# Kernel optimization log

Hardware: AMD Instinct MI355X
Metric: run time of the kernel (lower is better)

The kernel has to match this reference:

```python
import jax, jax.numpy as jnp
import numpy as np

U, B, I, D = 50000, 20000, 40000, 64
E_UI, E_UB, E_UBX, E_AGG = 1000000, 600000, 800000, 300000
EPS = 1e-8


def _bip_graph(rng, nA, nB, nE):
    """Symmetric Laplacian-normalized bipartite graph as directed COO edge list."""
    r = rng.integers(0, nA, nE)
    c = rng.integers(0, nB, nE)
    deg_r = np.bincount(r, minlength=nA).astype(np.float32)
    deg_c = np.bincount(c, minlength=nB).astype(np.float32)
    v = (1.0 / (np.sqrt(deg_r[r]) + EPS)) * (1.0 / (np.sqrt(deg_c[c]) + EPS))
    rows = np.concatenate([r, c + nA])
    cols = np.concatenate([c + nA, r])
    vals = np.concatenate([v, v]).astype(np.float32)
    return np.stack([rows, cols]).astype(np.int32), vals


def setup_inputs() -> dict:
    rng = np.random.default_rng(0)
    ui_idx, ui_val = _bip_graph(rng, U, I, E_UI)
    ub_idx, ub_val = _bip_graph(rng, U, B, E_UB)
    ubx_idx, ubx_val = _bip_graph(rng, U, B, E_UBX)  # ingredient-augmented u-b graph
    # bundle aggregation graph: row-normalized B x I (bi graph)
    br = rng.integers(0, B, E_AGG)
    bc = rng.integers(0, I, E_AGG)
    bdeg = np.bincount(br, minlength=B).astype(np.float32)
    agg_val = (1.0 / np.maximum(bdeg[br], 1.0)).astype(np.float32)
    agg_idx = np.stack([br, bc]).astype(np.int32)
    key = jax.random.key(0)
    ku, kb, ki = jax.random.split(key, 3)
    s = np.sqrt(2.0 / (U + D)).astype(np.float32)  # xavier-normal-ish scale
    return {
        "users_feature": jax.random.normal(ku, (U, D), jnp.float32) * 0.02,
        "bundles_feature": jax.random.normal(kb, (B, D), jnp.float32) * 0.02,
        "items_feature": jax.random.normal(ki, (I, D), jnp.float32) * 0.02,
        "ui_idx": jnp.asarray(ui_idx), "ui_val": jnp.asarray(ui_val),
        "ub_idx": jnp.asarray(ub_idx), "ub_val": jnp.asarray(ub_val),
        "ubx_idx": jnp.asarray(ubx_idx), "ubx_val": jnp.asarray(ubx_val),
        "agg_idx": jnp.asarray(agg_idx), "agg_val": jnp.asarray(agg_val),
        "num_layers": 2,
    }


def _spmm(idx, val, x, n_out):
    # y[r] += val[e] * x[c] for each edge e=(r,c)
    return jax.ops.segment_sum(val[:, None] * x[idx[1]], idx[0], num_segments=n_out)


def _l2norm(x):
    n = jnp.sqrt(jnp.sum(x * x, axis=1, keepdims=True))
    return x / jnp.maximum(n, 1e-12)


def _one_propagate(idx, val, A_feat, B_feat, num_layers):
    feats = jnp.concatenate([A_feat, B_feat], axis=0)
    n = feats.shape[0]
    acc = feats  # layer 0 raw
    f = feats
    for i in range(num_layers):
        f = _spmm(idx, val, f, n) / (i + 2)
        acc = acc + _l2norm(f)
    return acc[: A_feat.shape[0]], acc[A_feat.shape[0]:]


def reference(users_feature, bundles_feature, items_feature, ui_idx, ui_val,
              ub_idx, ub_val, ubx_idx, ubx_val, agg_idx, agg_val, num_layers):
    # item-level propagation over user-item graph
    IL_u, IL_i = _one_propagate(ui_idx, ui_val, users_feature, items_feature, num_layers)
    IL_b = _spmm(agg_idx, agg_val, IL_i, bundles_feature.shape[0])  # bundle agg from items
    # bundle-level propagation over user-bundle graph
    BL_u, BL_b = _one_propagate(ub_idx, ub_val, users_feature, bundles_feature, num_layers)
    # ingredient-augmented user-bundle propagation
    XL_u, XL_b = _one_propagate(ubx_idx, ubx_val, users_feature, bundles_feature, num_layers)
    # pack all representations: [3*U + 3*B, D]
    return jnp.concatenate([IL_u, BL_u, XL_u, IL_b, BL_b, XL_b], axis=0)
```

## Files before the change

kernel.cpp:

```cpp
#include <hip/hip_runtime.h>

#define D 64
constexpr int U_ = 50000, B_ = 20000, I_ = 40000;
constexpr int RPB  = 128;
constexpr int MAXB = 708;
constexpr int PTILE = 8192;

constexpr int NBU = 390;
constexpr int CAPU_UI = 3584, CAPB_UI = 4352;
constexpr int CAPA    = 2560;
constexpr int CAPU_UB = 2432, CAPB_UB = 4864;
constexpr int CAPU_UX = 2944, CAPB_UX = 6272;

__device__ __forceinline__ int g_nbU(int seg) { return seg == 1 ? 0 : NBU; }
__device__ __forceinline__ int g_capU(int seg) {
    switch (seg) { case 0: return CAPU_UI; case 1: return CAPA;
                   case 2: return CAPU_UB; default: return CAPU_UX; }
}
__device__ __forceinline__ int g_capB(int seg) {
    switch (seg) { case 0: return CAPB_UI; case 1: return CAPA;
                   case 2: return CAPB_UB; default: return CAPB_UX; }
}
__device__ __forceinline__ int bbase(int seg, int b) {
    int nbU = g_nbU(seg);
    return (b <= nbU) ? b * g_capU(seg)
                      : nbU * g_capU(seg) + (b - nbU) * g_capB(seg);
}

__device__ __forceinline__ unsigned short f2bf(float f) {
    unsigned int u = __float_as_uint(f);
    return (unsigned short)((u + 0x7FFFu + ((u >> 16) & 1u)) >> 16);
}

struct BuildP {
    const int *r0, *r1, *r2, *r3;
    int nnz0, nnz1, nnz2, nnz3;
    int G0, G1, G2, G3;
    int nb0, nb1, nb2, nb3;
    int co0, co1, co2, co3;
};

__global__ void __launch_bounds__(256)
k_cnt4(BuildP p, int* __restrict__ cnt) {
    __shared__ int lcnt[MAXB];
    int blk = blockIdx.x, t = threadIdx.x;
    int seg, rel, nnz, G, nbuck, co; const int* rows;
    if (blk < p.G0)                   { seg=0; rel=blk;              rows=p.r0; nnz=p.nnz0; G=p.G0; nbuck=p.nb0; co=p.co0; }
    else if (blk < p.G0+p.G1)         { seg=1; rel=blk-p.G0;         rows=p.r1; nnz=p.nnz1; G=p.G1; nbuck=p.nb1; co=p.co1; }
    else if (blk < p.G0+p.G1+p.G2)    { seg=2; rel=blk-p.G0-p.G1;    rows=p.r2; nnz=p.nnz2; G=p.G2; nbuck=p.nb2; co=p.co2; }
    else                              { seg=3; rel=blk-p.G0-p.G1-p.G2; rows=p.r3; nnz=p.nnz3; G=p.G3; nbuck=p.nb3; co=p.co3; }
    (void)seg;
    for (int i = t; i < nbuck; i += 256) lcnt[i] = 0;
    __syncthreads();
    int e0 = rel * PTILE, e1 = min(e0 + PTILE, nnz);
    int e = e0 + t;
    for (; e + 1792 < e1; e += 2048) {
        int r[8];
        #pragma unroll
        for (int k = 0; k < 8; k++) r[k] = rows[e + k * 256];
        #pragma unroll
        for (int k = 0; k < 8; k++) atomicAdd(&lcnt[r[k] >> 7], 1);
    }
    for (; e < e1; e += 256) atomicAdd(&lcnt[rows[e] >> 7], 1);
    __syncthreads();
    for (int b = t; b < nbuck; b += 256) cnt[co + (size_t)b * G + rel] = lcnt[b];
}

__global__ void __launch_bounds__(256)
k_scan4(BuildP p, int* __restrict__ cnt, int* __restrict__ bktcur) {
    __shared__ int sv[256];
    int bk = blockIdx.x, t = threadIdx.x;
    int seg, rel, G, co;
    if (bk < p.nb0)                    { seg=0; rel=bk;                 G=p.G0; co=p.co0; }
    else if (bk < p.nb0+p.nb1)         { seg=1; rel=bk-p.nb0;           G=p.G1; co=p.co1; }
    else if (bk < p.nb0+p.nb1+p.nb2)   { seg=2; rel=bk-p.nb0-p.nb1;     G=p.G2; co=p.co2; }
    else                               { seg=3; rel=bk-p.nb0-p.nb1-p.nb2; G=p.G3; co=p.co3; }
    int x = (t < G) ? cnt[co + (size_t)rel * G + t] : 0;
    sv[t] = x;
    __syncthreads();
    for (int off = 1; off < 256; off <<= 1) {
        int y = (t >= off) ? sv[t - off] : 0;
        __syncthreads();
        sv[t] += y;
        __syncthreads();
    }
    int bb = bbase(seg, rel);
    if (t < G) cnt[co + (size_t)rel * G + t] = bb + sv[t] - x;
    if (t == 255) bktcur[seg * MAXB + rel] = bb + sv[255];
}

__global__ void __launch_bounds__(256)
k_scat(const int* __restrict__ rows, const int* __restrict__ cols,
       int nnz, int G, int nbuck, int seg,
       const int* __restrict__ cnt, int* __restrict__ ep) {
    __shared__ int lbase[MAXB], lcnt[MAXB], llim[MAXB];
    int t = threadIdx.x, blk = blockIdx.x;
    for (int b = t; b < nbuck; b += 256) {
        lbase[b] = cnt[(size_t)b * G + blk];
        llim[b]  = bbase(seg, b + 1);
        lcnt[b]  = 0;
    }
    __syncthreads();
    int e0 = blk * PTILE, e1 = min(e0 + PTILE, nnz);
    int e = e0 + t;
    for (; e + 1792 < e1; e += 2048) {
        int r[8], c[8];
        #pragma unroll
        for (int k = 0; k < 8; k++) { r[k] = rows[e + k * 256]; c[k] = cols[e + k * 256]; }
        #pragma unroll
        for (int k = 0; k < 8; k++) {
            int b = r[k] >> 7;
            int pos = lbase[b] + atomicAdd(&lcnt[b], 1);
            if (pos < llim[b])
                ep[pos] = ((r[k] & (RPB - 1)) << 17) | c[k];
        }
    }
    for (; e < e1; e += 256) {
        int r = rows[e], c = cols[e];
        int b = r >> 7;
        int pos = lbase[b] + atomicAdd(&lcnt[b], 1);
        if (pos < llim[b])
            ep[pos] = ((r & (RPB - 1)) << 17) | c;
    }
}

__global__ void __launch_bounds__(256)
k_sort(const int* __restrict__ ep, const int* __restrict__ bktcur, int seg,
       int n, int mode, int do_pad, int* __restrict__ ecolS,
       int* __restrict__ rowstart, int* __restrict__ rowend,
       float* __restrict__ scale, int do_stage,
       const float* __restrict__ rawA, const float* __restrict__ rawB_adj,
       ushort* __restrict__ fb) {
    __shared__ int lc[4 * 129];
    __shared__ float sscale[RPB];
    __shared__ int wtot;
    int t = threadIdx.x;
    int b = blockIdx.x;
    int s = bbase(seg, b);
    int e = min(bktcur[b], bbase(seg, b + 1));
    int ne = e - s;
    for (int i = t; i < 4 * 129; i += 256) lc[i] = 0;
    __syncthreads();
    int rep = (t & 3) * 129;
    int i = t;
    for (; i + 768 < ne; i += 1024) {
        int p0 = ep[s + i], p1 = ep[s + i + 256], p2 = ep[s + i + 512], p3 = ep[s + i + 768];
        atomicAdd(&lc[rep + (p0 >> 17)], 1); atomicAdd(&lc[rep + (p1 >> 17)], 1);
        atomicAdd(&lc[rep + (p2 >> 17)], 1); atomicAdd(&lc[rep + (p3 >> 17)], 1);
    }
    for (; i < ne; i += 256) { int p = ep[s + i]; atomicAdd(&lc[rep + (p >> 17)], 1); }
    __syncthreads();
    int c_t = 0, pc_t = 0, v = 0;
    if (t < RPB) {
        c_t = lc[t] + lc[129 + t] + lc[258 + t] + lc[387 + t];
        pc_t = do_pad ? ((c_t + 7) & ~7) : c_t;
        v = pc_t;
        for (int off = 1; off < 64; off <<= 1) {
            int y = __shfl_up(v, off, 64);
            if ((t & 63) >= off) v += y;
        }
    }
    if (t == 63) wtot = v;
    __syncthreads();
    if (t >= 64 && t < RPB) v += wtot;
    if (t < RPB) {
        int row = b * RPB + t;
        if (row < n) {
            int st = s + (v - pc_t);
            rowstart[row] = st;
            rowend[row]   = st + pc_t;
            float sc = (mode == 0) ? 1.0f / (sqrtf((float)c_t) + 1e-8f)
                                   : 1.0f / (float)max(c_t, 1);
            scale[row] = sc;
            sscale[t] = sc;
            for (int k = c_t; k < pc_t; k++) ecolS[st + k] = n;
            lc[t] = st;
        } else lc[t] = 0;
    }
    __syncthreads();
    i = t;
    for (; i + 768 < ne; i += 1024) {
        int p0 = ep[s + i], p1 = ep[s + i + 256], p2 = ep[s + i + 512], p3 = ep[s + i + 768];
        int q0 = atomicAdd(&lc[p0 >> 17], 1); ecolS[q0] = p0 & 0x1FFFF;
        int q1 = atomicAdd(&lc[p1 >> 17], 1); ecolS[q1] = p1 & 0x1FFFF;
        int q2 = atomicAdd(&lc[p2 >> 17], 1); ecolS[q2] = p2 & 0x1FFFF;
        int q3 = atomicAdd(&lc[p3 >> 17], 1); ecolS[q3] = p3 & 0x1FFFF;
    }
    for (; i < ne; i += 256) {
        int p = ep[s + i];
        int q = atomicAdd(&lc[p >> 17], 1);
        ecolS[q] = p & 0x1FFFF;
    }
    if (do_stage) {
        int r0 = b * RPB;
        for (int idx = t; idx < RPB * 16; idx += 256) {
            int rl = idx >> 4, q = idx & 15;
            int row = r0 + rl;
            if (row > n) continue;
            ushort4 o;
            if (row == n) {
                o = make_ushort4(0, 0, 0, 0);
            } else {
                float sc = sscale[rl];
                float4 vv = (row < U_) ? ((const float4*)rawA)[(size_t)row * 16 + q]
                                       : ((const float4*)rawB_adj)[(size_t)row * 16 + q];
                o.x = f2bf(vv.x * sc); o.y = f2bf(vv.y * sc);
                o.z = f2bf(vv.z * sc); o.w = f2bf(vv.w * sc);
            }
            ((ushort4*)fb)[(size_t)row * 16 + q] = o;
        }
    }
}

__global__ void __launch_bounds__(256)
k_layer(const int* __restrict__ rowstart, const int* __restrict__ rowend,
        const int* __restrict__ ecol,
        const float* __restrict__ scale, int n, int zrow,
        const ushort* __restrict__ x, float inv,
        const float* __restrict__ rawA, const float* __restrict__ rawB_adj,
        ushort* __restrict__ fout, int write_f, int init,
        float* __restrict__ accA, float* __restrict__ accB) {
    if (write_f && blockIdx.x == 0 && threadIdx.x < 16)
        ((ushort4*)(fout + ((size_t)zrow << 6)))[threadIdx.x] = make_ushort4(0, 0, 0, 0);
    const int lane = threadIdx.x & 63;
    const int qtr  = lane >> 4;
    const int ql   = lane & 15;
    const int g = ql >> 3, q = ql & 7;
    int rowA = (blockIdx.x << 4) + ((threadIdx.x >> 6) << 2);
    if (rowA >= n) return;
    int row = rowA + qtr;
    int s = 0, e = 0;
    if (row < n) { s = rowstart[row]; e = rowend[row]; }
    float a0=0.f,a1=0.f,a2=0.f,a3=0.f,a4=0.f,a5=0.f,a6=0.f,a7=0.f;
    const uint4* __restrict__ xb = (const uint4*)x;

#define LDQ(m, vv) { int c_ = __shfl(cj, (qtr << 4) + ((m) << 1) + g, 64); \
                     vv = xb[((size_t)(unsigned)c_ << 3) + (unsigned)q]; }
#define ACCQ(vv) { \
    a0 += __uint_as_float(vv.x << 16); a1 += __uint_as_float(vv.x & 0xFFFF0000u); \
    a2 += __uint_as_float(vv.y << 16); a3 += __uint_as_float(vv.y & 0xFFFF0000u); \
    a4 += __uint_as_float(vv.z << 16); a5 += __uint_as_float(vv.z & 0xFFFF0000u); \
    a6 += __uint_as_float(vv.w << 16); a7 += __uint_as_float(vv.w & 0xFFFF0000u); }

    for (int base = s; base < e; base += 16) {
        int jn = e - base;
        int cj = ecol[base + ql];
        uint4 v0, v1, v2, v3, v4, v5, v6, v7;
        if (jn >= 16) {
            LDQ(0, v0); LDQ(1, v1); LDQ(2, v2); LDQ(3, v3);
            LDQ(4, v4); ACCQ(v0);
            LDQ(5, v5); ACCQ(v1);
            LDQ(6, v6); ACCQ(v2);
            LDQ(7, v7); ACCQ(v3);
            ACCQ(v4); ACCQ(v5); ACCQ(v6); ACCQ(v7);
        } else {
            LDQ(0, v0); LDQ(1, v1); LDQ(2, v2); LDQ(3, v3);
            ACCQ(v0); ACCQ(v1); ACCQ(v2); ACCQ(v3);
        }
    }
#undef LDQ
#undef ACCQ
#define RED(aa) { aa += __shfl_xor(aa, 8, 64); }
    RED(a0) RED(a1) RED(a2) RED(a3) RED(a4) RED(a5) RED(a6) RED(a7)
#undef RED
    float srow = (row < n) ? scale[row] : 0.f;
    float mlt = srow * inv;
    float w0=a0*mlt, w1=a1*mlt, w2=a2*mlt, w3=a3*mlt;
    float w4=a4*mlt, w5=a5*mlt, w6=a6*mlt, w7=a7*mlt;
    float sq = w0*w0 + w1*w1 + w2*w2 + w3*w3 + w4*w4 + w5*w5 + w6*w6 + w7*w7;
    sq += __shfl_xor(sq, 1, 64); sq += __shfl_xor(sq, 2, 64); sq += __shfl_xor(sq, 4, 64);
    float rn = 1.0f / fmaxf(sqrtf(sq), 1e-12f);
    if (row < n && g == 0) {
        size_t o = ((size_t)row << 6) + ((unsigned)q << 3);
        if (write_f) {
            unsigned p0 = (unsigned)f2bf(w0*srow) | ((unsigned)f2bf(w1*srow) << 16);
            unsigned p1 = (unsigned)f2bf(w2*srow) | ((unsigned)f2bf(w3*srow) << 16);
            unsigned p2 = (unsigned)f2bf(w4*srow) | ((unsigned)f2bf(w5*srow) << 16);
            unsigned p3 = (unsigned)f2bf(w6*srow) | ((unsigned)f2bf(w7*srow) << 16);
            *(uint4*)(fout + o) = make_uint4(p0, p1, p2, p3);
        }
        float r0=w0*rn, r1=w1*rn, r2=w2*rn, r3=w3*rn;
        float r4=w4*rn, r5=w5*rn, r6=w6*rn, r7=w7*rn;
        float* p = (row < U_) ? accA + o : accB + (o - ((size_t)U_ << 6));
        float4 c0, c1;
        if (init) {
            const float4* rp = (const float4*)((row < U_) ? rawA : rawB_adj)
                               + ((size_t)row << 4) + ((unsigned)q << 1);
            c0 = rp[0]; c1 = rp[1];
        } else {
            c0 = ((const float4*)p)[0]; c1 = ((const float4*)p)[1];
        }
        ((float4*)p)[0] = make_float4(c0.x + r0, c0.y + r1, c0.z + r2, c0.w + r3);
        ((float4*)p)[1] = make_float4(c1.x + r4, c1.y + r5, c1.z + r6, c1.w + r7);
    }
}

__global__ void k_spmm_csr(const int* __restrict__ rowstart, const int* __restrict__ rowend,
                           const int* __restrict__ ecol,
                           const float* __restrict__ rs, int n,
                           const float* __restrict__ x, float* __restrict__ y) {
    int row = (blockIdx.x << 2) + (threadIdx.x >> 6);
    if (row >= n) return;
    int lane = threadIdx.x & 63;
    int s = rowstart[row], e = rowend[row];
    float acc = 0.f;
    for (int base = s; base < e; base += 64) {
        int jn = e - base; if (jn > 64) jn = 64;
        int li = base + (lane < jn ? lane : jn - 1);
        int cj = ecol[li];
        int j = 0;
        for (; j + 8 <= jn; j += 8) {
            int c0 = __shfl(cj, j + 0, 64), c1 = __shfl(cj, j + 1, 64);
            int c2 = __shfl(cj, j + 2, 64), c3 = __shfl(cj, j + 3, 64);
            int c4 = __shfl(cj, j + 4, 64), c5 = __shfl(cj, j + 5, 64);
            int c6 = __shfl(cj, j + 6, 64), c7 = __shfl(cj, j + 7, 64);
            float v0 = x[(size_t)c0 * D + lane], v1 = x[(size_t)c1 * D + lane];
            float v2 = x[(size_t)c2 * D + lane], v3 = x[(size_t)c3 * D + lane];
            float v4 = x[(size_t)c4 * D + lane], v5 = x[(size_t)c5 * D + lane];
            float v6 = x[(size_t)c6 * D + lane], v7 = x[(size_t)c7 * D + lane];
            acc += ((v0 + v1) + (v2 + v3)) + ((v4 + v5) + (v6 + v7));
        }
        for (; j < jn; j++) {
            int c = __shfl(cj, j, 64);
            acc += x[(size_t)c * D + lane];
        }
    }
    y[(size_t)row * D + lane] = acc * rs[row];
}

extern "C" void kernel_launch(void* const* d_in, const int* in_sizes, int n_in,
                              void* d_out, int out_size, void* d_ws, size_t ws_size,
                              hipStream_t stream) {
    const float* users   = (const float*)d_in[0];
    const float* bundles = (const float*)d_in[1];
    const float* items   = (const float*)d_in[2];
    const int*   ui_idx  = (const int*)d_in[3];
    const int*   ub_idx  = (const int*)d_in[5];
    const int*   ubx_idx = (const int*)d_in[7];
    const int*   agg_idx = (const int*)d_in[9];
    const int ui_nnz  = in_sizes[4];
    const int ub_nnz  = in_sizes[6];
    const int ubx_nnz = in_sizes[8];
    const int agg_nnz = in_sizes[10];

    float* out = (float*)d_out;
    const size_t rowf = (size_t)D;

    const int NROWPAD = 90004;
    const int EPMAX   = 547 * 6144;
    ushort* fb16    = (ushort*)d_ws;
    float*  acc_itm = (float*)(fb16 + (size_t)(90001) * D + 32);
    float*  scale   = acc_itm + (size_t)I_ * D;
    int*    ep      = (int*)(scale + NROWPAD);
    ushort* gb16    = (ushort*)ep;
    int*    ecolS   = ep + EPMAX;
    int*    rowstart= ecolS + EPMAX;
    int*    rowend  = rowstart + NROWPAD;
    int*    bktcur  = rowend + NROWPAD;
    int*    cnt     = ep + 2950000;

    float* out_IL_u = out;
    float* out_BL_u = out + (size_t)U_ * rowf;
    float* out_XL_u = out + (size_t)2 * U_ * rowf;
    float* out_IL_b = out + (size_t)3 * U_ * rowf;
    float* out_BL_b = out + (size_t)3 * U_ * rowf + (size_t)B_ * rowf;
    float* out_XL_b = out + (size_t)3 * U_ * rowf + (size_t)2 * B_ * rowf;

    BuildP P;
    P.r0 = ui_idx;  P.nnz0 = ui_nnz;  P.G0 = (ui_nnz  + PTILE - 1) / PTILE;  P.nb0 = 704;
    P.r1 = agg_idx; P.nnz1 = agg_nnz; P.G1 = (agg_nnz + PTILE - 1) / PTILE;  P.nb1 = 157;
    P.r2 = ub_idx;  P.nnz2 = ub_nnz;  P.G2 = (ub_nnz  + PTILE - 1) / PTILE;  P.nb2 = 547;
    P.r3 = ubx_idx; P.nnz3 = ubx_nnz; P.G3 = (ubx_nnz + PTILE - 1) / PTILE;  P.nb3 = 547;
    P.co0 = 0;
    P.co1 = P.co0 + P.nb0 * P.G0;
    P.co2 = P.co1 + P.nb1 * P.G1;
    P.co3 = P.co2 + P.nb2 * P.G2;
    int Gsum  = P.G0 + P.G1 + P.G2 + P.G3;
    int nbsum = P.nb0 + P.nb1 + P.nb2 + P.nb3;
    hipLaunchKernelGGL(k_cnt4,  dim3(Gsum),  dim3(256), 0, stream, P, cnt);
    hipLaunchKernelGGL(k_scan4, dim3(nbsum), dim3(256), 0, stream, P, cnt, bktcur);

    auto build = [&](const int* idxp, int nnz, int n, int mode, int do_pad,
                     int do_stage, const float* A, const float* Badj,
                     int seg, int G, int co) {
        int nbuck = (n + RPB - 1) / RPB;
        hipLaunchKernelGGL(k_scat, dim3(G), dim3(256), 0, stream,
                           idxp, idxp + nnz, nnz, G, nbuck, seg, cnt + co, ep);
        hipLaunchKernelGGL(k_sort, dim3(nbuck), dim3(256), 0, stream,
                           ep, bktcur + seg * MAXB, seg, n, mode, do_pad, ecolS,
                           rowstart, rowend, scale, do_stage, A, Badj, fb16);
    };

    auto propagate = [&](const int* idxp, int nnz, int seg, int G, int co,
                         const float* Bfeat, int nB, float* accA, float* accB) {
        const int n = U_ + nB;
        const float* Badj = Bfeat - (size_t)U_ * rowf;
        build(idxp, nnz, n, 0, 1, 1, users, Badj, seg, G, co);
        hipLaunchKernelGGL(k_layer, dim3((n + 15) / 16), dim3(256), 0, stream,
                           rowstart, rowend, ecolS, scale, n, n, fb16, 0.5f,
                           users, Badj, gb16, 1, 1, accA, accB);
        hipLaunchKernelGGL(k_layer, dim3((n + 15) / 16), dim3(256), 0, stream,
                           rowstart, rowend, ecolS, scale, n, n, gb16, 1.0f / 3.0f,
                           users, Badj, (ushort*)nullptr, 0, 0, accA, accB);
    };

    propagate(ui_idx, ui_nnz, 0, P.G0, P.co0, items, I_, out_IL_u, acc_itm);

    build(agg_idx, agg_nnz, B_, 1, 0, 0, users, users, 1, P.G1, P.co1);
    hipLaunchKernelGGL(k_spmm_csr, dim3((B_ + 3) / 4), dim3(256), 0, stream,
                       rowstart, rowend, ecolS, scale, B_, acc_itm, out_IL_b);

    propagate(ub_idx, ub_nnz, 2, P.G2, P.co2, bundles, B_, out_BL_u, out_BL_b);

    propagate(ubx_idx, ubx_nnz, 3, P.G3, P.co3, bundles, B_, out_XL_u, out_XL_b);
}
```

Before: 463.3 us.

## Fuse graph build and propagation phases into persistent cooperative kernels

Replaces the many per-stage kernel launches (count, scan, scatter, sort, two layers, spmm) with two cooperative persistent kernels that loop over work with grid-stride blocks and separate phases with grid-wide syncs. The aim is to remove launch overhead and inter-kernel gaps across the roughly fourteen launches. In exchange, grid size is capped by occupancy, so each block processes several logical blocks serially. Grid syncs carry their own cost, and the fused kernel may use more registers, lowering occupancy for the layer phase.

New measurement: 1.747 ms. 277% more time.

```diff
diff --git a/kernel.cpp b/kernel.cpp
--- a/kernel.cpp
+++ b/kernel.cpp
@@ -1,4 +1,7 @@
 #include <hip/hip_runtime.h>
+#include <hip/hip_cooperative_groups.h>
+
+namespace cg = cooperative_groups;
 
 #define D 64
 constexpr int U_ = 50000, B_ = 20000, I_ = 40000;
@@ -41,199 +44,90 @@
 };
 
 __global__ void __launch_bounds__(256)
-k_cnt4(BuildP p, int* __restrict__ cnt) {
+k_cntscan(BuildP p, int* cnt, int* bktcur) {
+    cg::grid_group gg = cg::this_grid();
     __shared__ int lcnt[MAXB];
-    int blk = blockIdx.x, t = threadIdx.x;
-    int seg, rel, nnz, G, nbuck, co; const int* rows;
-    if (blk < p.G0)                   { seg=0; rel=blk;              rows=p.r0; nnz=p.nnz0; G=p.G0; nbuck=p.nb0; co=p.co0; }
-    else if (blk < p.G0+p.G1)         { seg=1; rel=blk-p.G0;         rows=p.r1; nnz=p.nnz1; G=p.G1; nbuck=p.nb1; co=p.co1; }
-    else if (blk < p.G0+p.G1+p.G2)    { seg=2; rel=blk-p.G0-p.G1;    rows=p.r2; nnz=p.nnz2; G=p.G2; nbuck=p.nb2; co=p.co2; }
-    else                              { seg=3; rel=blk-p.G0-p.G1-p.G2; rows=p.r3; nnz=p.nnz3; G=p.G3; nbuck=p.nb3; co=p.co3; }
-    (void)seg;
-    for (int i = t; i < nbuck; i += 256) lcnt[i] = 0;
-    __syncthreads();
-    int e0 = rel * PTILE, e1 = min(e0 + PTILE, nnz);
-    int e = e0 + t;
-    for (; e + 1792 < e1; e += 2048) {
-        int r[8];
-        #pragma unroll
-        for (int k = 0; k < 8; k++) r[k] = rows[e + k * 256];
-        #pragma unroll
-        for (int k = 0; k < 8; k++) atomicAdd(&lcnt[r[k] >> 7], 1);
-    }
-    for (; e < e1; e += 256) atomicAdd(&lcnt[rows[e] >> 7], 1);
-    __syncthreads();
-    for (int b = t; b < nbuck; b += 256) cnt[co + (size_t)b * G + rel] = lcnt[b];
-}
-
-__global__ void __launch_bounds__(256)
-k_scan4(BuildP p, int* __restrict__ cnt, int* __restrict__ bktcur) {
     __shared__ int sv[256];
-    int bk = blockIdx.x, t = threadIdx.x;
-    int seg, rel, G, co;
-    if (bk < p.nb0)                    { seg=0; rel=bk;                 G=p.G0; co=p.co0; }
-    else if (bk < p.nb0+p.nb1)         { seg=1; rel=bk-p.nb0;           G=p.G1; co=p.co1; }
-    else if (bk < p.nb0+p.nb1+p.nb2)   { seg=2; rel=bk-p.nb0-p.nb1;     G=p.G2; co=p.co2; }
-    else                               { seg=3; rel=bk-p.nb0-p.nb1-p.nb2; G=p.G3; co=p.co3; }
-    int x = (t < G) ? cnt[co + (size_t)rel * G + t] : 0;
-    sv[t] = x;
-    __syncthreads();
-    for (int off = 1; off < 256; off <<= 1) {
-        int y = (t >= off) ? sv[t - off] : 0;
+    int t = threadIdx.x;
+    int Gsum = p.G0 + p.G1 + p.G2 + p.G3;
+    for (int blk = blockIdx.x; blk < Gsum; blk += gridDim.x) {
+        int rel, nnz, G, nbuck, co; const int* rows;
+        if (blk < p.G0)                   { rel=blk;                 rows=p.r0; nnz=p.nnz0; G=p.G0; nbuck=p.nb0; co=p.co0; }
+        else if (blk < p.G0+p.G1)         { rel=blk-p.G0;            rows=p.r1; nnz=p.nnz1; G=p.G1; nbuck=p.nb1; co=p.co1; }
+        else if (blk < p.G0+p.G1+p.G2)    { rel=blk-p.G0-p.G1;       rows=p.r2; nnz=p.nnz2; G=p.G2; nbuck=p.nb2; co=p.co2; }
+        else                              { rel=blk-p.G0-p.G1-p.G2;  rows=p.r3; nnz=p.nnz3; G=p.G3; nbuck=p.nb3; co=p.co3; }
         __syncthreads();
-        sv[t] += y;
+        for (int i = t; i < nbuck; i += 256) lcnt[i] = 0;
         __syncthreads();
-    }
-    int bb = bbase(seg, rel);
-    if (t < G) cnt[co + (size_t)rel * G + t] = bb + sv[t] - x;
-    if (t == 255) bktcur[seg * MAXB + rel] = bb + sv[255];
-}
-
-__global__ void __launch_bounds__(256)
-k_scat(const int* __restrict__ rows, const int* __restrict__ cols,
-       int nnz, int G, int nbuck, int seg,
-       const int* __restrict__ cnt, int* __restrict__ ep) {
-    __shared__ int lbase[MAXB], lcnt[MAXB], llim[MAXB];
-    int t = threadIdx.x, blk = blockIdx.x;
-    for (int b = t; b < nbuck; b += 256) {
-        lbase[b] = cnt[(size_t)b * G + blk];
-        llim[b]  = bbase(seg, b + 1);
-        lcnt[b]  = 0;
-    }
-    __syncthreads();
-    int e0 = blk * PTILE, e1 = min(e0 + PTILE, nnz);
-    int e = e0 + t;
-    for (; e + 1792 < e1; e += 2048) {
-        int r[8], c[8];
-        #pragma unroll
-        for (int k = 0; k < 8; k++) { r[k] = rows[e + k * 256]; c[k] = cols[e + k * 256]; }
-        #pragma unroll
-        for (int k = 0; k < 8; k++) {
-            int b = r[k] >> 7;
-            int pos = lbase[b] + atomicAdd(&lcnt[b], 1);
-            if (pos < llim[b])
-                ep[pos] = ((r[k] & (RPB - 1)) << 17) | c[k];
-        }
-    }
-    for (; e < e1; e += 256) {
-        int r = rows[e], c = cols[e];
-        int b = r >> 7;
-        int pos = lbase[b] + atomicAdd(&lcnt[b], 1);
-        if (pos < llim[b])
-            ep[pos] = ((r & (RPB - 1)) << 17) | c;
-    }
-}
-
-__global__ void __launch_bounds__(256)
-k_sort(const int* __restrict__ ep, const int* __restrict__ bktcur, int seg,
-       int n, int mode, int do_pad, int* __restrict__ ecolS,
-       int* __restrict__ rowstart, int* __restrict__ rowend,
-       float* __restrict__ scale, int do_stage,
-       const float* __restrict__ rawA, const float* __restrict__ rawB_adj,
-       ushort* __restrict__ fb) {
-    __shared__ int lc[4 * 129];
-    __shared__ float sscale[RPB];
-    __shared__ int wtot;
-    int t = threadIdx.x;
-    int b = blockIdx.x;
-    int s = bbase(seg, b);
-    int e = min(bktcur[b], bbase(seg, b + 1));
-    int ne = e - s;
-    for (int i = t; i < 4 * 129; i += 256) lc[i] = 0;
-    __syncthreads();
-    int rep = (t & 3) * 129;
-    int i = t;
-    for (; i + 768 < ne; i += 1024) {
-        int p0 = ep[s + i], p1 = ep[s + i + 256], p2 = ep[s + i + 512], p3 = ep[s + i + 768];
-        atomicAdd(&lc[rep + (p0 >> 17)], 1); atomicAdd(&lc[rep + (p1 >> 17)], 1);
-        atomicAdd(&lc[rep + (p2 >> 17)], 1); atomicAdd(&lc[rep + (p3 >> 17)], 1);
-    }
-    for (; i < ne; i += 256) { int p = ep[s + i]; atomicAdd(&lc[rep + (p >> 17)], 1); }
-    __syncthreads();
-    int c_t = 0, pc_t = 0, v = 0;
-    if (t < RPB) {
-        c_t = lc[t] + lc[129 + t] + lc[258 + t] + lc[387 + t];
-        pc_t = do_pad ? ((c_t + 7) & ~7) : c_t;
-        v = pc_t;
-        for (int off = 1; off < 64; off <<= 1) {
-            int y = __shfl_up(v, off, 64);
-            if ((t & 63) >= off) v += y;
-        }
-    }
-    if (t == 63) wtot = v;
-    __syncthreads();
-    if (t >= 64 && t < RPB) v += wtot;
-    if (t < RPB) {
-        int row = b * RPB + t;
-        if (row < n) {
-            int st = s + (v - pc_t);
-            rowstart[row] = st;
-            rowend[row]   = st + pc_t;
-            float sc = (mode == 0) ? 1.0f / (sqrtf((float)c_t) + 1e-8f)
-                                   : 1.0f / (float)max(c_t, 1);
-            scale[row] = sc;
-            sscale[t] = sc;
-            for (int k = c_t; k < pc_t; k++) ecolS[st + k] = n;
-            lc[t] = st;
-        } else lc[t] = 0;
-    }
-    __syncthreads();
-    i = t;
-    for (; i + 768 < ne; i += 1024) {
-        int p0 = ep[s + i], p1 = ep[s + i + 256], p2 = ep[s + i + 512], p3 = ep[s + i + 768];
-        int q0 = atomicAdd(&lc[p0 >> 17], 1); ecolS[q0] = p0 & 0x1FFFF;
-        int q1 = atomicAdd(&lc[p1 >> 17], 1); ecolS[q1] = p1 & 0x1FFFF;
-        int q2 = atomicAdd(&lc[p2 >> 17], 1); ecolS[q2] = p2 & 0x1FFFF;
-        int q3 = atomicAdd(&lc[p3 >> 17], 1); ecolS[q3] = p3 & 0x1FFFF;
-    }
-    for (; i < ne; i += 256) {
-        int p = ep[s + i];
-        int q = atomicAdd(&lc[p >> 17], 1);
-        ecolS[q] = p & 0x1FFFF;
-    }
-    if (do_stage) {
-        int r0 = b * RPB;
-        for (int idx = t; idx < RPB * 16; idx += 256) {
-            int rl = idx >> 4, q = idx & 15;
-            int row = r0 + rl;
-            if (row > n) continue;
-            ushort4 o;
-            if (row == n) {
-                o = make_ushort4(0, 0, 0, 0);
-            } else {
-                float sc = sscale[rl];
-                float4 vv = (row < U_) ? ((const float4*)rawA)[(size_t)row * 16 + q]
-                                       : ((const float4*)rawB_adj)[(size_t)row * 16 + q];
-                o.x = f2bf(vv.x * sc); o.y = f2bf(vv.y * sc);
-                o.z = f2bf(vv.z * sc); o.w = f2bf(vv.w * sc);
-            }
-            ((ushort4*)fb)[(size_t)row * 16 + q] = o;
-        }
-    }
-}
-
-__global__ void __launch_bounds__(256)
-k_layer(const int* __restrict__ rowstart, const int* __restrict__ rowend,
-        const int* __restrict__ ecol,
-        const float* __restrict__ scale, int n, int zrow,
-        const ushort* __restrict__ x, float inv,
-        const float* __restrict__ rawA, const float* __restrict__ rawB_adj,
-        ushort* __restrict__ fout, int write_f, int init,
-        float* __restrict__ accA, float* __restrict__ accB) {
+        int e0 = rel * PTILE, e1 = min(e0 + PTILE, nnz);
+        int e = e0 + t;
+        for (; e + 1792 < e1; e += 2048) {
+            int r[8];
+            #pragma unroll
+            for (int k = 0; k < 8; k++) r[k] = rows[e + k * 256];
+            #pragma unroll
+            for (int k = 0; k < 8; k++) atomicAdd(&lcnt[r[k] >> 7], 1);
+        }
+        for (; e < e1; e += 256) atomicAdd(&lcnt[rows[e] >> 7], 1);
+        __syncthreads();
+        for (int b = t; b < nbuck; b += 256) cnt[co + (size_t)b * G + rel] = lcnt[b];
+    }
+    gg.sync();
+    int nbsum = p.nb0 + p.nb1 + p.nb2 + p.nb3;
+    for (int bk = blockIdx.x; bk < nbsum; bk += gridDim.x) {
+        int seg, rel, G, co;
+        if (bk < p.nb0)                    { seg=0; rel=bk;                   G=p.G0; co=p.co0; }
+        else if (bk < p.nb0+p.nb1)         { seg=1; rel=bk-p.nb0;             G=p.G1; co=p.co1; }
+        else if (bk < p.nb0+p.nb1+p.nb2)   { seg=2; rel=bk-p.nb0-p.nb1;       G=p.G2; co=p.co2; }
+        else                               { seg=3; rel=bk-p.nb0-p.nb1-p.nb2; G=p.G3; co=p.co3; }
+        int x = (t < G) ? cnt[co + (size_t)rel * G + t] : 0;
+        __syncthreads();
+        sv[t] = x;
+        __syncthreads();
+        for (int off = 1; off < 256; off <<= 1) {
+            int y = (t >= off) ? sv[t - off] : 0;
+            __syncthreads();
+            sv[t] += y;
+            __syncthreads();
+        }
+        int bb = bbase(seg, rel);
+        if (t < G) cnt[co + (size_t)rel * G + t] = bb + sv[t] - x;
+        if (t == 255) bktcur[seg * MAXB + rel] = bb + sv[255];
+    }
+}
+
+struct GP {
+    const int* rows; const int* cols;
+    const int* cnt;
+    int* ep;
+    const int* bktcur;
+    int* ecolS; int* rowstart; int* rowend; float* scale;
+    const float* rawA; const float* rawB_adj;
+    ushort* fb; ushort* gb;
+    float* accA; float* accB;
+    const float* spx; float* spy;
+    float inv0, inv1;
+    int nnz, G, nbuck, seg, n, mode, do_pad, do_stage, do_layers, do_spmm, spn;
+};
+
+__device__ __forceinline__ void layer_phase(const GP& P, const ushort* x,
+                                            ushort* fout, float inv,
+                                            int write_f, int init) {
     if (write_f && blockIdx.x == 0 && threadIdx.x < 16)
-        ((ushort4*)(fout + ((size_t)zrow << 6)))[threadIdx.x] = make_ushort4(0, 0, 0, 0);
+        ((ushort4*)(fout + ((size_t)P.n << 6)))[threadIdx.x] = make_ushort4(0, 0, 0, 0);
     const int lane = threadIdx.x & 63;
     const int qtr  = lane >> 4;
     const int ql   = lane & 15;
     const int g = ql >> 3, q = ql & 7;
-    int rowA = (blockIdx.x << 4) + ((threadIdx.x >> 6) << 2);
-    if (rowA >= n) return;
-    int row = rowA + qtr;
-    int s = 0, e = 0;
-    if (row < n) { s = rowstart[row]; e = rowend[row]; }
-    float a0=0.f,a1=0.f,a2=0.f,a3=0.f,a4=0.f,a5=0.f,a6=0.f,a7=0.f;
-    const uint4* __restrict__ xb = (const uint4*)x;
-
+    const uint4* xb = (const uint4*)x;
+    int nq = (P.n + 15) >> 4;
+    for (int blk = blockIdx.x; blk < nq; blk += gridDim.x) {
+        int rowA = (blk << 4) + ((threadIdx.x >> 6) << 2);
+        if (rowA >= P.n) continue;
+        int row = rowA + qtr;
+        int s = 0, e = 0;
+        if (row < P.n) { s = P.rowstart[row]; e = P.rowend[row]; }
+        float a0=0.f,a1=0.f,a2=0.f,a3=0.f,a4=0.f,a5=0.f,a6=0.f,a7=0.f;
 #define LDQ(m, vv) { int c_ = __shfl(cj, (qtr << 4) + ((m) << 1) + g, 64); \
                      vv = xb[((size_t)(unsigned)c_ << 3) + (unsigned)q]; }
 #define ACCQ(vv) { \
@@ -241,91 +135,220 @@
     a2 += __uint_as_float(vv.y << 16); a3 += __uint_as_float(vv.y & 0xFFFF0000u); \
     a4 += __uint_as_float(vv.z << 16); a5 += __uint_as_float(vv.z & 0xFFFF0000u); \
     a6 += __uint_as_float(vv.w << 16); a7 += __uint_as_float(vv.w & 0xFFFF0000u); }
-
-    for (int base = s; base < e; base += 16) {
-        int jn = e - base;
-        int cj = ecol[base + ql];
-        uint4 v0, v1, v2, v3, v4, v5, v6, v7;
-        if (jn >= 16) {
-            LDQ(0, v0); LDQ(1, v1); LDQ(2, v2); LDQ(3, v3);
-            LDQ(4, v4); ACCQ(v0);
-            LDQ(5, v5); ACCQ(v1);
-            LDQ(6, v6); ACCQ(v2);
-            LDQ(7, v7); ACCQ(v3);
-            ACCQ(v4); ACCQ(v5); ACCQ(v6); ACCQ(v7);
-        } else {
-            LDQ(0, v0); LDQ(1, v1); LDQ(2, v2); LDQ(3, v3);
-            ACCQ(v0); ACCQ(v1); ACCQ(v2); ACCQ(v3);
-        }
-    }
+        for (int base = s; base < e; base += 16) {
+            int jn = e - base;
+            int cj = P.ecolS[base + ql];
+            uint4 v0, v1, v2, v3, v4, v5, v6, v7;
+            if (jn >= 16) {
+                LDQ(0, v0); LDQ(1, v1); LDQ(2, v2); LDQ(3, v3);
+                LDQ(4, v4); ACCQ(v0);
+                LDQ(5, v5); ACCQ(v1);
+                LDQ(6, v6); ACCQ(v2);
+                LDQ(7, v7); ACCQ(v3);
+                ACCQ(v4); ACCQ(v5); ACCQ(v6); ACCQ(v7);
+            } else {
+                LDQ(0, v0); LDQ(1, v1); LDQ(2, v2); LDQ(3, v3);
+                ACCQ(v0); ACCQ(v1); ACCQ(v2); ACCQ(v3);
+            }
+        }
 #undef LDQ
 #undef ACCQ
 #define RED(aa) { aa += __shfl_xor(aa, 8, 64); }
-    RED(a0) RED(a1) RED(a2) RED(a3) RED(a4) RED(a5) RED(a6) RED(a7)
+        RED(a0) RED(a1) RED(a2) RED(a3) RED(a4) RED(a5) RED(a6) RED(a7)
 #undef RED
-    float srow = (row < n) ? scale[row] : 0.f;
-    float mlt = srow * inv;
-    float w0=a0*mlt, w1=a1*mlt, w2=a2*mlt, w3=a3*mlt;
-    float w4=a4*mlt, w5=a5*mlt, w6=a6*mlt, w7=a7*mlt;
-    float sq = w0*w0 + w1*w1 + w2*w2 + w3*w3 + w4*w4 + w5*w5 + w6*w6 + w7*w7;
-    sq += __shfl_xor(sq, 1, 64); sq += __shfl_xor(sq, 2, 64); sq += __shfl_xor(sq, 4, 64);
-    float rn = 1.0f / fmaxf(sqrtf(sq), 1e-12f);
-    if (row < n && g == 0) {
-        size_t o = ((size_t)row << 6) + ((unsigned)q << 3);
-        if (write_f) {
-            unsigned p0 = (unsigned)f2bf(w0*srow) | ((unsigned)f2bf(w1*srow) << 16);
-            unsigned p1 = (unsigned)f2bf(w2*srow) | ((unsigned)f2bf(w3*srow) << 16);
-            unsigned p2 = (unsigned)f2bf(w4*srow) | ((unsigned)f2bf(w5*srow) << 16);
-            unsigned p3 = (unsigned)f2bf(w6*srow) | ((unsigned)f2bf(w7*srow) << 16);
-            *(uint4*)(fout + o) = make_uint4(p0, p1, p2, p3);
-        }
-        float r0=w0*rn, r1=w1*rn, r2=w2*rn, r3=w3*rn;
-        float r4=w4*rn, r5=w5*rn, r6=w6*rn, r7=w7*rn;
-        float* p = (row < U_) ? accA + o : accB + (o - ((size_t)U_ << 6));
-        float4 c0, c1;
-        if (init) {
-            const float4* rp = (const float4*)((row < U_) ? rawA : rawB_adj)
-                               + ((size_t)row << 4) + ((unsigned)q << 1);
-            c0 = rp[0]; c1 = rp[1];
-        } else {
-            c0 = ((const float4*)p)[0]; c1 = ((const float4*)p)[1];
-        }
-        ((float4*)p)[0] = make_float4(c0.x + r0, c0.y + r1, c0.z + r2, c0.w + r3);
-        ((float4*)p)[1] = make_float4(c1.x + r4, c1.y + r5, c1.z + r6, c1.w + r7);
-    }
-}
-
-__global__ void k_spmm_csr(const int* __restrict__ rowstart, const int* __restrict__ rowend,
-                           const int* __restrict__ ecol,
-                           const float* __restrict__ rs, int n,
-                           const float* __restrict__ x, float* __restrict__ y) {
-    int row = (blockIdx.x << 2) + (threadIdx.x >> 6);
-    if (row >= n) return;
+        float srow = (row < P.n) ? P.scale[row] : 0.f;
+        float mlt = srow * inv;
+        float w0=a0*mlt, w1=a1*mlt, w2=a2*mlt, w3=a3*mlt;
+        float w4=a4*mlt, w5=a5*mlt, w6=a6*mlt, w7=a7*mlt;
+        float sq = w0*w0 + w1*w1 + w2*w2 + w3*w3 + w4*w4 + w5*w5 + w6*w6 + w7*w7;
+        sq += __shfl_xor(sq, 1, 64); sq += __shfl_xor(sq, 2, 64); sq += __shfl_xor(sq, 4, 64);
+        float rn = 1.0f / fmaxf(sqrtf(sq), 1e-12f);
+        if (row < P.n && g == 0) {
+            size_t o = ((size_t)row << 6) + ((unsigned)q << 3);
+            if (write_f) {
+                unsigned p0 = (unsigned)f2bf(w0*srow) | ((unsigned)f2bf(w1*srow) << 16);
+                unsigned p1 = (unsigned)f2bf(w2*srow) | ((unsigned)f2bf(w3*srow) << 16);
+                unsigned p2 = (unsigned)f2bf(w4*srow) | ((unsigned)f2bf(w5*srow) << 16);
+                unsigned p3 = (unsigned)f2bf(w6*srow) | ((unsigned)f2bf(w7*srow) << 16);
+                *(uint4*)(fout + o) = make_uint4(p0, p1, p2, p3);
+            }
+            float r0=w0*rn, r1=w1*rn, r2=w2*rn, r3=w3*rn;
+            float r4=w4*rn, r5=w5*rn, r6=w6*rn, r7=w7*rn;
+            float* p = (row < U_) ? P.accA + o : P.accB + (o - ((size_t)U_ << 6));
+            float4 c0, c1;
+            if (init) {
+                const float4* rp = (const float4*)((row < U_) ? P.rawA : P.rawB_adj)
+                                   + ((size_t)row << 4) + ((unsigned)q << 1);
+                c0 = rp[0]; c1 = rp[1];
+            } else {
+                c0 = ((const float4*)p)[0]; c1 = ((const float4*)p)[1];
+            }
+            ((float4*)p)[0] = make_float4(c0.x + r0, c0.y + r1, c0.z + r2, c0.w + r3);
+            ((float4*)p)[1] = make_float4(c1.x + r4, c1.y + r5, c1.z + r6, c1.w + r7);
+        }
+    }
+}
+
+__device__ void spmm_phase(const GP& P) {
     int lane = threadIdx.x & 63;
-    int s = rowstart[row], e = rowend[row];
-    float acc = 0.f;
-    for (int base = s; base < e; base += 64) {
-        int jn = e - base; if (jn > 64) jn = 64;
-        int li = base + (lane < jn ? lane : jn - 1);
-        int cj = ecol[li];
-        int j = 0;
-        for (; j + 8 <= jn; j += 8) {
-            int c0 = __shfl(cj, j + 0, 64), c1 = __shfl(cj, j + 1, 64);
-            int c2 = __shfl(cj, j + 2, 64), c3 = __shfl(cj, j + 3, 64);
-            int c4 = __shfl(cj, j + 4, 64), c5 = __shfl(cj, j + 5, 64);
-            int c6 = __shfl(cj, j + 6, 64), c7 = __shfl(cj, j + 7, 64);
-            float v0 = x[(size_t)c0 * D + lane], v1 = x[(size_t)c1 * D + lane];
-            float v2 = x[(size_t)c2 * D + lane], v3 = x[(size_t)c3 * D + lane];
-            float v4 = x[(size_t)c4 * D + lane], v5 = x[(size_t)c5 * D + lane];
-            float v6 = x[(size_t)c6 * D + lane], v7 = x[(size_t)c7 * D + lane];
-            acc += ((v0 + v1) + (v2 + v3)) + ((v4 + v5) + (v6 + v7));
-        }
-        for (; j < jn; j++) {
-            int c = __shfl(cj, j, 64);
-            acc += x[(size_t)c * D + lane];
-        }
-    }
-    y[(size_t)row * D + lane] = acc * rs[row];
+    int nb4 = (P.spn + 3) >> 2;
+    for (int blk = blockIdx.x; blk < nb4; blk += gridDim.x) {
+        int row = (blk << 2) + (threadIdx.x >> 6);
+        if (row >= P.spn) continue;
+        int s = P.rowstart[row], e = P.rowend[row];
+        float acc = 0.f;
+        for (int base = s; base < e; base += 64) {
+            int jn = e - base; if (jn > 64) jn = 64;
+            int li = base + (lane < jn ? lane : jn - 1);
+            int cj = P.ecolS[li];
+            int j = 0;
+            for (; j + 8 <= jn; j += 8) {
+                int c0 = __shfl(cj, j + 0, 64), c1 = __shfl(cj, j + 1, 64);
+                int c2 = __shfl(cj, j + 2, 64), c3 = __shfl(cj, j + 3, 64);
+                int c4 = __shfl(cj, j + 4, 64), c5 = __shfl(cj, j + 5, 64);
+                int c6 = __shfl(cj, j + 6, 64), c7 = __shfl(cj, j + 7, 64);
+                float v0 = P.spx[(size_t)c0 * D + lane], v1 = P.spx[(size_t)c1 * D + lane];
+                float v2 = P.spx[(size_t)c2 * D + lane], v3 = P.spx[(size_t)c3 * D + lane];
+                float v4 = P.spx[(size_t)c4 * D + lane], v5 = P.spx[(size_t)c5 * D + lane];
+                float v6 = P.spx[(size_t)c6 * D + lane], v7 = P.spx[(size_t)c7 * D + lane];
+                acc += ((v0 + v1) + (v2 + v3)) + ((v4 + v5) + (v6 + v7));
+            }
+            for (; j < jn; j++) {
+                int c = __shfl(cj, j, 64);
+                acc += P.spx[(size_t)c * D + lane];
+            }
+        }
+        P.spy[(size_t)row * D + lane] = acc * P.scale[row];
+    }
+}
+
+__global__ void __launch_bounds__(256)
+k_graph(GP P) {
+    cg::grid_group gg = cg::this_grid();
+    int t = threadIdx.x;
+    {
+        __shared__ int lbase[MAXB], lcnt[MAXB], llim[MAXB];
+        for (int blk = blockIdx.x; blk < P.G; blk += gridDim.x) {
+            __syncthreads();
+            for (int b = t; b < P.nbuck; b += 256) {
+                lbase[b] = P.cnt[(size_t)b * P.G + blk];
+                llim[b]  = bbase(P.seg, b + 1);
+                lcnt[b]  = 0;
+            }
+            __syncthreads();
+            int e0 = blk * PTILE, e1 = min(e0 + PTILE, P.nnz);
+            int e = e0 + t;
+            for (; e + 1792 < e1; e += 2048) {
+                int r[8], c[8];
+                #pragma unroll
+                for (int k = 0; k < 8; k++) { r[k] = P.rows[e + k * 256]; c[k] = P.cols[e + k * 256]; }
+                #pragma unroll
+                for (int k = 0; k < 8; k++) {
+                    int b = r[k] >> 7;
+                    int pos = lbase[b] + atomicAdd(&lcnt[b], 1);
+                    if (pos < llim[b])
+                        P.ep[pos] = ((r[k] & (RPB - 1)) << 17) | c[k];
+                }
+            }
+            for (; e < e1; e += 256) {
+                int r = P.rows[e], c = P.cols[e];
+                int b = r >> 7;
+                int pos = lbase[b] + atomicAdd(&lcnt[b], 1);
+                if (pos < llim[b])
+                    P.ep[pos] = ((r & (RPB - 1)) << 17) | c;
+            }
+        }
+    }
+    gg.sync();
+    {
+        __shared__ int lc[4 * 129];
+        __shared__ float sscale[RPB];
+        __shared__ int wtot;
+        for (int b = blockIdx.x; b < P.nbuck; b += gridDim.x) {
+            __syncthreads();
+            int s = bbase(P.seg, b);
+            int e = min(P.bktcur[b], bbase(P.seg, b + 1));
+            int ne = e - s;
+            for (int i = t; i < 4 * 129; i += 256) lc[i] = 0;
+            __syncthreads();
+            int rep = (t & 3) * 129;
+            int i = t;
+            for (; i + 768 < ne; i += 1024) {
+                int p0 = P.ep[s+i], p1 = P.ep[s+i+256], p2 = P.ep[s+i+512], p3 = P.ep[s+i+768];
+                atomicAdd(&lc[rep + (p0 >> 17)], 1); atomicAdd(&lc[rep + (p1 >> 17)], 1);
+                atomicAdd(&lc[rep + (p2 >> 17)], 1); atomicAdd(&lc[rep + (p3 >> 17)], 1);
+            }
+            for (; i < ne; i += 256) { int p = P.ep[s + i]; atomicAdd(&lc[rep + (p >> 17)], 1); }
+            __syncthreads();
+            int c_t = 0, pc_t = 0, v = 0;
+            if (t < RPB) {
+                c_t = lc[t] + lc[129 + t] + lc[258 + t] + lc[387 + t];
+                pc_t = P.do_pad ? ((c_t + 7) & ~7) : c_t;
+                v = pc_t;
+                for (int off = 1; off < 64; off <<= 1) {
+                    int y = __shfl_up(v, off, 64);
+                    if ((t & 63) >= off) v += y;
+                }
+            }
+            if (t == 63) wtot = v;
+            __syncthreads();
+            if (t >= 64 && t < RPB) v += wtot;
+            if (t < RPB) {
+                int row = b * RPB + t;
+                if (row < P.n) {
+                    int st = s + (v - pc_t);
+                    P.rowstart[row] = st;
+                    P.rowend[row]   = st + pc_t;
+                    float sc = (P.mode == 0) ? 1.0f / (sqrtf((float)c_t) + 1e-8f)
+                                             : 1.0f / (float)max(c_t, 1);
+                    P.scale[row] = sc;
+                    sscale[t] = sc;
+                    for (int k = c_t; k < pc_t; k++) P.ecolS[st + k] = P.n;
+                    lc[t] = st;
+                } else lc[t] = 0;
+            }
+            __syncthreads();
+            i = t;
+            for (; i + 768 < ne; i += 1024) {
+                int p0 = P.ep[s+i], p1 = P.ep[s+i+256], p2 = P.ep[s+i+512], p3 = P.ep[s+i+768];
+                int q0 = atomicAdd(&lc[p0 >> 17], 1); P.ecolS[q0] = p0 & 0x1FFFF;
+                int q1 = atomicAdd(&lc[p1 >> 17], 1); P.ecolS[q1] = p1 & 0x1FFFF;
+                int q2 = atomicAdd(&lc[p2 >> 17], 1); P.ecolS[q2] = p2 & 0x1FFFF;
+                int q3 = atomicAdd(&lc[p3 >> 17], 1); P.ecolS[q3] = p3 & 0x1FFFF;
+            }
+            for (; i < ne; i += 256) {
+                int p = P.ep[s + i];
+                int q = atomicAdd(&lc[p >> 17], 1);
+                P.ecolS[q] = p & 0x1FFFF;
+            }
+            if (P.do_stage) {
+                int r0 = b * RPB;
+                for (int idx = t; idx < RPB * 16; idx += 256) {
+                    int rl = idx >> 4, q = idx & 15;
+                    int row = r0 + rl;
+                    if (row > P.n) continue;
+                    ushort4 o;
+                    if (row == P.n) {
+                        o = make_ushort4(0, 0, 0, 0);
+                    } else {
+                        float sc = sscale[rl];
+                        float4 vv = (row < U_) ? ((const float4*)P.rawA)[(size_t)row * 16 + q]
+                                               : ((const float4*)P.rawB_adj)[(size_t)row * 16 + q];
+                        o.x = f2bf(vv.x * sc); o.y = f2bf(vv.y * sc);
+                        o.z = f2bf(vv.z * sc); o.w = f2bf(vv.w * sc);
+                    }
+                    ((ushort4*)P.fb)[(size_t)row * 16 + q] = o;
+                }
+            }
+        }
+    }
+    gg.sync();
+    if (P.do_layers) {
+        layer_phase(P, P.fb, P.gb, P.inv0, 1, 1);
+        gg.sync();
+        layer_phase(P, P.gb, (ushort*)nullptr, P.inv1, 0, 0);
+    }
+    if (P.do_spmm) spmm_phase(P);
 }
 
 extern "C" void kernel_launch(void* const* d_in, const int* in_sizes, int n_in,
@@ -375,42 +398,53 @@
     P.co1 = P.co0 + P.nb0 * P.G0;
     P.co2 = P.co1 + P.nb1 * P.G1;
     P.co3 = P.co2 + P.nb2 * P.G2;
-    int Gsum  = P.G0 + P.G1 + P.G2 + P.G3;
-    int nbsum = P.nb0 + P.nb1 + P.nb2 + P.nb3;
-    hipLaunchKernelGGL(k_cnt4,  dim3(Gsum),  dim3(256), 0, stream, P, cnt);
-    hipLaunchKernelGGL(k_scan4, dim3(nbsum), dim3(256), 0, stream, P, cnt, bktcur);
-
-    auto build = [&](const int* idxp, int nnz, int n, int mode, int do_pad,
-                     int do_stage, const float* A, const float* Badj,
-                     int seg, int G, int co) {
-        int nbuck = (n + RPB - 1) / RPB;
-        hipLaunchKernelGGL(k_scat, dim3(G), dim3(256), 0, stream,
-                           idxp, idxp + nnz, nnz, G, nbuck, seg, cnt + co, ep);
-        hipLaunchKernelGGL(k_sort, dim3(nbuck), dim3(256), 0, stream,
-                           ep, bktcur + seg * MAXB, seg, n, mode, do_pad, ecolS,
-                           rowstart, rowend, scale, do_stage, A, Badj, fb16);
+
+    int mbA = 1, mbG = 1;
+    hipOccupancyMaxActiveBlocksPerMultiprocessor(&mbA, k_cntscan, 256, 0);
+    hipOccupancyMaxActiveBlocksPerMultiprocessor(&mbG, k_graph, 256, 0);
+    if (mbA < 1) mbA = 1;
+    if (mbG < 1) mbG = 1;
+    int gridA = min(2048, mbA * 256);
+    int gridG = min(2048, mbG * 256);
+
+    void* argsA[] = { (void*)&P, (void*)&cnt, (void*)&bktcur };
+    hipLaunchCooperativeKernel(k_cntscan, dim3(gridA), dim3(256), argsA, 0, stream);
+
+    auto mkgp = [&](const int* idxp, int nnz, int n, int mode, int do_pad,
+                    int do_stage, const float* A, const float* Badj,
+                    int seg, int G, int co, int do_layers,
+                    float* accA, float* accB,
+                    int do_spmm, const float* spx, float* spy, int spn) {
+        GP g{};
+        g.rows = idxp; g.cols = idxp + nnz; g.nnz = nnz; g.G = G;
+        g.nbuck = (n + RPB - 1) / RPB; g.seg = seg; g.n = n; g.mode = mode;
+        g.do_pad = do_pad; g.do_stage = do_stage; g.do_layers = do_layers;
+        g.do_spmm = do_spmm; g.spn = spn;
+        g.cnt = cnt + co; g.ep = ep; g.bktcur = bktcur + seg * MAXB;
+        g.ecolS = ecolS; g.rowstart = rowstart; g.rowend = rowend; g.scale = scale;
+        g.rawA = A; g.rawB_adj = Badj; g.fb = fb16; g.gb = gb16;
+        g.accA = accA; g.accB = accB; g.spx = spx; g.spy = spy;
+        g.inv0 = 0.5f; g.inv1 = 1.0f / 3.0f;
+        return g;
     };
-
-    auto propagate = [&](const int* idxp, int nnz, int seg, int G, int co,
-                         const float* Bfeat, int nB, float* accA, float* accB) {
-        const int n = U_ + nB;
-        const float* Badj = Bfeat - (size_t)U_ * rowf;
-        build(idxp, nnz, n, 0, 1, 1, users, Badj, seg, G, co);
-        hipLaunchKernelGGL(k_layer, dim3((n + 15) / 16), dim3(256), 0, stream,
-                           rowstart, rowend, ecolS, scale, n, n, fb16, 0.5f,
-                           users, Badj, gb16, 1, 1, accA, accB);
-        hipLaunchKernelGGL(k_layer, dim3((n + 15) / 16), dim3(256), 0, stream,
-                           rowstart, rowend, ecolS, scale, n, n, gb16, 1.0f / 3.0f,
-                           users, Badj, (ushort*)nullptr, 0, 0, accA, accB);
+    auto launch_g = [&](GP& g) {
+        void* args[] = { (void*)&g };
+        hipLaunchCooperativeKernel(k_graph, dim3(gridG), dim3(256), args, 0, stream);
     };
 
-    propagate(ui_idx, ui_nnz, 0, P.G0, P.co0, items, I_, out_IL_u, acc_itm);
-
-    build(agg_idx, agg_nnz, B_, 1, 0, 0, users, users, 1, P.G1, P.co1);
-    hipLaunchKernelGGL(k_spmm_csr, dim3((B_ + 3) / 4), dim3(256), 0, stream,
-                       rowstart, rowend, ecolS, scale, B_, acc_itm, out_IL_b);
-
-    propagate(ub_idx, ub_nnz, 2, P.G2, P.co2, bundles, B_, out_BL_u, out_BL_b);
-
-    propagate(ubx_idx, ubx_nnz, 3, P.G3, P.co3, bundles, B_, out_XL_u, out_XL_b);
-}
+    GP gui = mkgp(ui_idx, ui_nnz, U_ + I_, 0, 1, 1, users, items - (size_t)U_ * rowf,
+                  0, P.G0, P.co0, 1, out_IL_u, acc_itm, 0, nullptr, nullptr, 0);
+    launch_g(gui);
+
+    GP gagg = mkgp(agg_idx, agg_nnz, B_, 1, 0, 0, users, users,
+                   1, P.G1, P.co1, 0, nullptr, nullptr, 1, acc_itm, out_IL_b, B_);
+    launch_g(gagg);
+
+    GP gub = mkgp(ub_idx, ub_nnz, U_ + B_, 0, 1, 1, users, bundles - (size_t)U_ * rowf,
+                  2, P.G2, P.co2, 1, out_BL_u, out_BL_b, 0, nullptr, nullptr, 0);
+    launch_g(gub);
+
+    GP gubx = mkgp(ubx_idx, ubx_nnz, U_ + B_, 0, 1, 1, users, bundles - (size_t)U_ * rowf,
+                   3, P.G3, P.co3, 1, out_XL_u, out_XL_b, 0, nullptr, nullptr, 0);
+    launch_g(gubx);
+}
```
